# Performance work log

Hardware: AMD Instinct MI355X
Metric: run time of the kernel (lower is better)

The kernel has to match this reference:

```python
import jax, jax.numpy as jnp
import numpy as np

B, T, N, F = 32, 4096, 11, 16
NUM_LABS = 20
H = 2 * F  # refine hidden dim
LN_EPS = 1e-5


def setup_inputs() -> dict:
    key = jax.random.key(0)
    ks = jax.random.split(key, 8)
    x = jax.random.normal(ks[0], (B, T, N, F), dtype=jnp.float32)
    lab_idx = jax.random.randint(ks[1], (B,), 0, NUM_LABS)
    # projection: identity + small noise, per lab
    projection = (jnp.eye(N, dtype=jnp.float32)[None].repeat(NUM_LABS, axis=0)
                  + 0.01 * jax.random.normal(ks[2], (NUM_LABS, N, N), dtype=jnp.float32))
    bias = jnp.zeros((NUM_LABS, 1, N, F), dtype=jnp.float32)
    w1 = jax.random.normal(ks[3], (F, H), dtype=jnp.float32) / np.sqrt(F)
    b1 = jnp.zeros((H,), dtype=jnp.float32)
    ln_g = jnp.ones((H,), dtype=jnp.float32)
    ln_b = jnp.zeros((H,), dtype=jnp.float32)
    w2 = jax.random.normal(ks[4], (H, F), dtype=jnp.float32) / np.sqrt(H)
    b2 = jnp.zeros((F,), dtype=jnp.float32)
    return {"x": x, "lab_idx": lab_idx, "projection": projection, "bias": bias,
            "w1": w1, "b1": b1, "ln_g": ln_g, "ln_b": ln_b, "w2": w2, "b2": b2}


def reference(x, lab_idx, projection, bias, w1, b1, ln_g, ln_b, w2, b2):
    # gather per-sample projection / bias by lab index
    W = projection[lab_idx]          # [b, n, n]
    Bb = bias[lab_idx]               # [b, 1, n, f]
    # torch: bmm(x^T, W) then transpose -> out[b,t,m,f] = sum_n x[b,t,n,f] * W[b,n,m]
    out = jnp.einsum('btnf,bnm->btmf', x, W) + Bb
    # refine MLP: Linear -> LayerNorm -> GELU(exact) -> Linear
    h = out @ w1 + b1                                    # [b,t,n,2f]
    mu = jnp.mean(h, axis=-1, keepdims=True)
    var = jnp.var(h, axis=-1, keepdims=True)
    h = (h - mu) / jnp.sqrt(var + LN_EPS) * ln_g + ln_b
    h = jax.nn.gelu(h, approximate=False)
    return h @ w2 + b2
```

## Files before the change

### kernel.cpp

```cpp
#include <hip/hip_runtime.h>
#include <hip/hip_bf16.h>
#include <math.h>

#define BB 32
#define TT 4096
#define NN 11
#define FF 16
#define HH 32
#define LN_EPS 1e-5f
#define TOTAL_ROWS (BB * TT * NN)
#define ROWS_PER_BLOCK 256
#define NBLOCKS (TOTAL_ROWS / ROWS_PER_BLOCK)
#define BLOCKS_PER_BATCH (TT * NN / ROWS_PER_BLOCK)

typedef __attribute__((ext_vector_type(8))) short short8;
typedef __attribute__((ext_vector_type(4))) float f32x4;

union Frag { unsigned u[4]; uint4 u4; short8 v; };

__device__ __forceinline__ unsigned pack2_bf16(float a, float b) {
    __hip_bfloat162 p = __float22bfloat162_rn(make_float2(a, b));
    union { __hip_bfloat162 h; unsigned u; } cvt; cvt.h = p; return cvt.u;
}

__device__ __forceinline__ float fast_gelu(float v) {
    const float v2 = v * v;
    const float c  = fmaf(0.044715f, v2, 1.0f);
    const float t  = v * c * 1.5957691216057308f;
    const float e  = __expf(-t);
    return v * __builtin_amdgcn_rcpf(1.0f + e);
}

__global__ __launch_bounds__(256) void fused_proj_mlp_t(
    const float* __restrict__ x,
    const int*   __restrict__ lab_idx,
    const float* __restrict__ proj,
    const float* __restrict__ bias,
    const float* __restrict__ w1,
    const float* __restrict__ b1,
    const float* __restrict__ ln_g,
    const float* __restrict__ ln_b,
    const float* __restrict__ w2,
    const float* __restrict__ b2,
    float*       __restrict__ out)
{
    __shared__ unsigned o_st[4][64][12];

    const int tid  = threadIdx.x;
    const int wv   = tid >> 6;
    const int lane = tid & 63;
    const int q    = lane >> 4;
    const int c    = lane & 15;

    const int row        = blockIdx.x * ROWS_PER_BLOCK + tid;
    const unsigned token = (unsigned)row / 11u;
    const int m          = row - (int)(token * 11u);
    const int lab        = lab_idx[blockIdx.x / BLOCKS_PER_BATCH];

    Frag a1c0, a1c1, a2f;
    #pragma unroll
    for (int d = 0; d < 4; ++d) {
        const int k0 = 8 * q + 2 * d;
        float wa0 = 0.f, wa1 = 0.f, wb0 = 0.f, wb1 = 0.f;
        if (q < 2) {
            wa0 = w1[k0 * HH + c];       wa1 = w1[(k0 + 1) * HH + c];
            wb0 = w1[k0 * HH + 16 + c];  wb1 = w1[(k0 + 1) * HH + 16 + c];
        }
        a1c0.u[d] = pack2_bf16(wa0, wa1);
        a1c1.u[d] = pack2_bf16(wb0, wb1);
        a2f.u[d]  = pack2_bf16(w2[k0 * FF + c], w2[(k0 + 1) * FF + c]);
    }

    float4 b1v0 = *reinterpret_cast<const float4*>(b1 + 4 * q);
    float4 b1v1 = *reinterpret_cast<const float4*>(b1 + 16 + 4 * q);
    float4 b2v  = *reinterpret_cast<const float4*>(b2 + 4 * q);
    float4 g0   = *reinterpret_cast<const float4*>(ln_g + 4 * q);
    float4 g1   = *reinterpret_cast<const float4*>(ln_g + 16 + 4 * q);
    float4 e0   = *reinterpret_cast<const float4*>(ln_b + 4 * q);
    float4 e1   = *reinterpret_cast<const float4*>(ln_b + 16 + 4 * q);
    float g0a[4] = {g0.x, g0.y, g0.z, g0.w}, g1a[4] = {g1.x, g1.y, g1.z, g1.w};
    float e0a[4] = {e0.x, e0.y, e0.z, e0.w}, e1a[4] = {e1.x, e1.y, e1.z, e1.w};
    float b1a0[4] = {b1v0.x, b1v0.y, b1v0.z, b1v0.w};
    float b1a1[4] = {b1v1.x, b1v1.y, b1v1.z, b1v1.w};
    float b2a[4]  = {b2v.x, b2v.y, b2v.z, b2v.w};

    const float4* xp4 = reinterpret_cast<const float4*>(x) + (size_t)token * (NN * FF / 4);
    const float*  Wp  = proj + (size_t)lab * (NN * NN) + m;
    const float4* bp4 = reinterpret_cast<const float4*>(bias) + (size_t)lab * (NN * FF / 4) + m * (FF / 4);

    float o[FF];
    #pragma unroll
    for (int f4 = 0; f4 < FF / 4; ++f4) {
        float4 v = bp4[f4];
        o[f4*4+0] = v.x; o[f4*4+1] = v.y; o[f4*4+2] = v.z; o[f4*4+3] = v.w;
    }
    #pragma unroll
    for (int n = 0; n < NN; ++n) {
        const float wnm = Wp[n * NN];
        #pragma unroll
        for (int f4 = 0; f4 < FF / 4; ++f4) {
            float4 v = xp4[n * (FF / 4) + f4];
            o[f4*4+0] = fmaf(v.x, wnm, o[f4*4+0]);
            o[f4*4+1] = fmaf(v.y, wnm, o[f4*4+1]);
            o[f4*4+2] = fmaf(v.z, wnm, o[f4*4+2]);
            o[f4*4+3] = fmaf(v.w, wnm, o[f4*4+3]);
        }
    }

    {
        unsigned p[8];
        #pragma unroll
        for (int d = 0; d < 8; ++d) p[d] = pack2_bf16(o[2*d], o[2*d+1]);
        uint4* dst = reinterpret_cast<uint4*>(&o_st[wv][lane][0]);
        dst[0] = make_uint4(p[0], p[1], p[2], p[3]);
        dst[1] = make_uint4(p[4], p[5], p[6], p[7]);
    }

    const int rowbase = blockIdx.x * ROWS_PER_BLOCK + wv * 64;
    const int srcA = (q & 1) * 32 + c;
    const int srcB = srcA + 16;

    #pragma unroll
    for (int tt = 0; tt < 4; ++tt) {
        Frag B1;
        B1.u4 = *reinterpret_cast<const uint4*>(&o_st[wv][tt * 16 + c][(q & 1) * 4]);

        f32x4 accA = { b1a0[0], b1a0[1], b1a0[2], b1a0[3] };
        f32x4 accB = { b1a1[0], b1a1[1], b1a1[2], b1a1[3] };
        accA = __builtin_amdgcn_mfma_f32_16x16x32_bf16(a1c0.v, B1.v, accA, 0, 0, 0);
        accB = __builtin_amdgcn_mfma_f32_16x16x32_bf16(a1c1.v, B1.v, accB, 0, 0, 0);

        float s = 0.f, ss = 0.f;
        #pragma unroll
        for (int i = 0; i < 4; ++i) {
            s += accA[i] + accB[i];
            ss = fmaf(accA[i], accA[i], ss);
            ss = fmaf(accB[i], accB[i], ss);
        }
        s  += __shfl_xor(s, 16, 64);  s  += __shfl_xor(s, 32, 64);
        ss += __shfl_xor(ss, 16, 64); ss += __shfl_xor(ss, 32, 64);
        const float mu   = s * (1.f / HH);
        const float var  = ss * (1.f / HH) - mu * mu;
        const float rstd = rsqrtf(var + LN_EPS);
        const float nb   = -mu * rstd;

        float ga[4], gb[4];
        #pragma unroll
        for (int i = 0; i < 4; ++i) {
            ga[i] = fast_gelu(fmaf(fmaf(accA[i], rstd, nb), g0a[i], e0a[i]));
            gb[i] = fast_gelu(fmaf(fmaf(accB[i], rstd, nb), g1a[i], e1a[i]));
        }
        const unsigned c0d0 = pack2_bf16(ga[0], ga[1]);
        const unsigned c0d1 = pack2_bf16(ga[2], ga[3]);
        const unsigned c1d0 = pack2_bf16(gb[0], gb[1]);
        const unsigned c1d1 = pack2_bf16(gb[2], gb[3]);

        Frag B2;
        {
            unsigned lo, hi;
            lo = __shfl((int)c0d0, srcA, 64); hi = __shfl((int)c1d0, srcA, 64);
            B2.u[0] = (q < 2) ? lo : hi;
            lo = __shfl((int)c0d1, srcA, 64); hi = __shfl((int)c1d1, srcA, 64);
            B2.u[1] = (q < 2) ? lo : hi;
            lo = __shfl((int)c0d0, srcB, 64); hi = __shfl((int)c1d0, srcB, 64);
            B2.u[2] = (q < 2) ? lo : hi;
            lo = __shfl((int)c0d1, srcB, 64); hi = __shfl((int)c1d1, srcB, 64);
            B2.u[3] = (q < 2) ? lo : hi;
        }

        f32x4 acc2 = { b2a[0], b2a[1], b2a[2], b2a[3] };
        acc2 = __builtin_amdgcn_mfma_f32_16x16x32_bf16(a2f.v, B2.v, acc2, 0, 0, 0);

        float4* dst = reinterpret_cast<float4*>(out + (size_t)(rowbase + tt * 16 + c) * FF + 4 * q);
        *dst = make_float4(acc2[0], acc2[1], acc2[2], acc2[3]);
    }
}

extern "C" void kernel_launch(void* const* d_in, const int* in_sizes, int n_in,
                              void* d_out, int out_size, void* d_ws, size_t ws_size,
                              hipStream_t stream) {
    const float* x       = (const float*)d_in[0];
    const int*   lab_idx = (const int*)  d_in[1];
    const float* proj    = (const float*)d_in[2];
    const float* bias    = (const float*)d_in[3];
    const float* w1      = (const float*)d_in[4];
    const float* b1      = (const float*)d_in[5];
    const float* ln_g    = (const float*)d_in[6];
    const float* ln_b    = (const float*)d_in[7];
    const float* w2      = (const float*)d_in[8];
    const float* b2      = (const float*)d_in[9];
    float* out = (float*)d_out;

    fused_proj_mlp_t<<<NBLOCKS, 256, 0, stream>>>(
        x, lab_idx, proj, bias, w1, b1, ln_g, ln_b, w2, b2, out);
}
```

Measured before the change: 231.6 us.

## Remap threads to token×f4 slices so each x element is loaded once

Before, each thread computed one output row (token, m) and re-read all 11 x rows of its token, so every x element was fetched 11 times across threads. Now each thread owns one token and one float4 slice of F. It loads its 11 x float4 values once, accumulates all 11 projected rows in registers, and writes them as bf16 to LDS with a 48-byte row stride. Each wave then runs 11 MFMA tiles over its own 176 rows. This cuts redundant global and L2 traffic, at the cost of more registers, a larger LDS footprint (about 33KB per block) and fewer blocks in the grid.

```diff
diff --git a/kernel.cpp b/kernel.cpp
--- a/kernel.cpp
+++ b/kernel.cpp
@@ -8,10 +8,11 @@
 #define FF 16
 #define HH 32
 #define LN_EPS 1e-5f
-#define TOTAL_ROWS (BB * TT * NN)
-#define ROWS_PER_BLOCK 256
-#define NBLOCKS (TOTAL_ROWS / ROWS_PER_BLOCK)
-#define BLOCKS_PER_BATCH (TT * NN / ROWS_PER_BLOCK)
+
+#define TOKENS_PER_BLOCK 64
+#define NBLOCKS (BB * TT / TOKENS_PER_BLOCK)
+#define BLOCKS_PER_BATCH (TT / TOKENS_PER_BLOCK)
+#define ROW_STRIDE_B 48
 
 typedef __attribute__((ext_vector_type(8))) short short8;
 typedef __attribute__((ext_vector_type(4))) float f32x4;
@@ -31,7 +32,7 @@
     return v * __builtin_amdgcn_rcpf(1.0f + e);
 }
 
-__global__ __launch_bounds__(256) void fused_proj_mlp_t(
+__global__ __launch_bounds__(256) void fused_v5(
     const float* __restrict__ x,
     const int*   __restrict__ lab_idx,
     const float* __restrict__ proj,
@@ -44,18 +45,18 @@
     const float* __restrict__ b2,
     float*       __restrict__ out)
 {
-    __shared__ unsigned o_st[4][64][12];
+    __shared__ __align__(16) unsigned char o_st[704 * ROW_STRIDE_B];
 
     const int tid  = threadIdx.x;
     const int wv   = tid >> 6;
     const int lane = tid & 63;
     const int q    = lane >> 4;
     const int c    = lane & 15;
+    const int tl   = tid >> 2;
+    const int f4   = tid & 3;
 
-    const int row        = blockIdx.x * ROWS_PER_BLOCK + tid;
-    const unsigned token = (unsigned)row / 11u;
-    const int m          = row - (int)(token * 11u);
-    const int lab        = lab_idx[blockIdx.x / BLOCKS_PER_BATCH];
+    const int token = blockIdx.x * TOKENS_PER_BLOCK + tl;
+    const int lab   = lab_idx[blockIdx.x / BLOCKS_PER_BATCH];
 
     Frag a1c0, a1c1, a2f;
     #pragma unroll
@@ -84,46 +85,46 @@
     float b1a1[4] = {b1v1.x, b1v1.y, b1v1.z, b1v1.w};
     float b2a[4]  = {b2v.x, b2v.y, b2v.z, b2v.w};
 
-    const float4* xp4 = reinterpret_cast<const float4*>(x) + (size_t)token * (NN * FF / 4);
-    const float*  Wp  = proj + (size_t)lab * (NN * NN) + m;
-    const float4* bp4 = reinterpret_cast<const float4*>(bias) + (size_t)lab * (NN * FF / 4) + m * (FF / 4);
+    const float4* xb = reinterpret_cast<const float4*>(x)    + (size_t)token * (NN * FF / 4) + f4;
+    const float4* bb = reinterpret_cast<const float4*>(bias) + (size_t)lab   * (NN * FF / 4) + f4;
+    const float*  Wl = proj + (size_t)lab * (NN * NN);
 
-    float o[FF];
+    float o[NN][4];
     #pragma unroll
-    for (int f4 = 0; f4 < FF / 4; ++f4) {
-        float4 v = bp4[f4];
-        o[f4*4+0] = v.x; o[f4*4+1] = v.y; o[f4*4+2] = v.z; o[f4*4+3] = v.w;
+    for (int m = 0; m < NN; ++m) {
+        float4 bv = bb[4 * m];
+        o[m][0] = bv.x; o[m][1] = bv.y; o[m][2] = bv.z; o[m][3] = bv.w;
     }
     #pragma unroll
     for (int n = 0; n < NN; ++n) {
-        const float wnm = Wp[n * NN];
+        float4 xv = xb[4 * n];
         #pragma unroll
-        for (int f4 = 0; f4 < FF / 4; ++f4) {
-            float4 v = xp4[n * (FF / 4) + f4];
-            o[f4*4+0] = fmaf(v.x, wnm, o[f4*4+0]);
-            o[f4*4+1] = fmaf(v.y, wnm, o[f4*4+1]);
-            o[f4*4+2] = fmaf(v.z, wnm, o[f4*4+2]);
-            o[f4*4+3] = fmaf(v.w, wnm, o[f4*4+3]);
+        for (int m = 0; m < NN; ++m) {
+            const float wm = Wl[n * NN + m];
+            o[m][0] = fmaf(xv.x, wm, o[m][0]);
+            o[m][1] = fmaf(xv.y, wm, o[m][1]);
+            o[m][2] = fmaf(xv.z, wm, o[m][2]);
+            o[m][3] = fmaf(xv.w, wm, o[m][3]);
         }
     }
 
-    {
-        unsigned p[8];
-        #pragma unroll
-        for (int d = 0; d < 8; ++d) p[d] = pack2_bf16(o[2*d], o[2*d+1]);
-        uint4* dst = reinterpret_cast<uint4*>(&o_st[wv][lane][0]);
-        dst[0] = make_uint4(p[0], p[1], p[2], p[3]);
-        dst[1] = make_uint4(p[4], p[5], p[6], p[7]);
+    #pragma unroll
+    for (int m = 0; m < NN; ++m) {
+        uint2 p;
+        p.x = pack2_bf16(o[m][0], o[m][1]);
+        p.y = pack2_bf16(o[m][2], o[m][3]);
+        *reinterpret_cast<uint2*>(&o_st[(tl * NN + m) * ROW_STRIDE_B + f4 * 8]) = p;
     }
 
-    const int rowbase = blockIdx.x * ROWS_PER_BLOCK + wv * 64;
+    const size_t outrow0 = (size_t)blockIdx.x * (TOKENS_PER_BLOCK * NN) + wv * 176;
     const int srcA = (q & 1) * 32 + c;
     const int srcB = srcA + 16;
 
     #pragma unroll
-    for (int tt = 0; tt < 4; ++tt) {
+    for (int t = 0; t < NN; ++t) {
         Frag B1;
-        B1.u4 = *reinterpret_cast<const uint4*>(&o_st[wv][tt * 16 + c][(q & 1) * 4]);
+        B1.u4 = *reinterpret_cast<const uint4*>(
+            &o_st[(176 * wv + 16 * t + c) * ROW_STRIDE_B + (q & 1) * 16]);
 
         f32x4 accA = { b1a0[0], b1a0[1], b1a0[2], b1a0[3] };
         f32x4 accB = { b1a1[0], b1a1[1], b1a1[2], b1a1[3] };
@@ -171,7 +172,7 @@
         f32x4 acc2 = { b2a[0], b2a[1], b2a[2], b2a[3] };
         acc2 = __builtin_amdgcn_mfma_f32_16x16x32_bf16(a2f.v, B2.v, acc2, 0, 0, 0);
 
-        float4* dst = reinterpret_cast<float4*>(out + (size_t)(rowbase + tt * 16 + c) * FF + 4 * q);
+        float4* dst = reinterpret_cast<float4*>(out + (outrow0 + 16 * t + c) * FF + 4 * q);
         *dst = make_float4(acc2[0], acc2[1], acc2[2], acc2[3]);
     }
 }
@@ -191,6 +192,6 @@
     const float* b2      = (const float*)d_in[9];
     float* out = (float*)d_out;
 
-    fused_proj_mlp_t<<<NBLOCKS, 256, 0, stream>>>(
+    fused_v5<<<NBLOCKS, 256, 0, stream>>>(
         x, lab_idx, proj, bias, w1, b1, ln_g, ln_b, w2, b2, out);
 }
```

Measured after the change: 200.3 us. -13.5%, faster.
